# Kernel tuning notes

Measured on AMD Instinct MI355X. Metric: run time of the kernel, lower is better.

Reference implementation:

```python
import jax, jax.numpy as jnp
import numpy as np

NEG_BIG = -1e12
ALPHA = 0.2  # LeakyReLU negative slope

def setup_inputs() -> dict:
    key = jax.random.key(0)
    k1, k2, k3, k4, k5 = jax.random.split(key, 5)
    N, F_in, F_out = 8192, 256, 128
    inp = jax.random.normal(k1, (N, F_in), dtype=jnp.float32)
    adj = jax.random.randint(k2, (N, N), 0, 2, dtype=jnp.int32)
    W = jax.random.normal(k3, (F_in, F_out), dtype=jnp.float32) * 0.05
    W_2 = jax.random.normal(k4, (F_in, F_out), dtype=jnp.float32) * 0.05
    W_3 = jax.random.normal(k5, (F_in, F_out), dtype=jnp.float32) * 0.05
    return {"inp": inp, "adj": adj, "W": W, "W_2": W_2, "W_3": W_3}

def reference(inp, adj, W, W_2, W_3):
    # h = inp @ W, h_2 = inp @ W_2  -> scores e = LeakyReLU(h @ h_2^T)  [N, N]
    h = inp @ W
    h_2 = inp @ W_2
    e = jax.nn.leaky_relu(h @ h_2.T, negative_slope=ALPHA)
    # adjacency mask, row softmax (dropout disabled: eval mode)
    attention = jax.nn.softmax(jnp.where(adj > 0, e, NEG_BIG), axis=1)
    h_3 = inp @ W_3
    h_prime = attention @ h_3
    return jax.nn.elu(h_prime)  # concat=True path
```

## Files before the change

kernel.cpp:

```cpp
#include <hip/hip_runtime.h>
#include <hip/hip_fp16.h>

#define N    8192
#define FIN  256
#define FOUT 128
#define BN   64

typedef _Float16 half8 __attribute__((ext_vector_type(8)));
typedef _Float16 half4v __attribute__((ext_vector_type(4)));
typedef float floatx4 __attribute__((ext_vector_type(4)));

__device__ __forceinline__ float exp2_fast(float x) { return __builtin_amdgcn_exp2f(x); }

__device__ __forceinline__ void gload_lds16(const void* g, void* l) {
    __builtin_amdgcn_global_load_lds(
        (const __attribute__((address_space(1))) void*)g,
        (__attribute__((address_space(3))) void*)l, 16, 0, 0);
}

__global__ __launch_bounds__(256)
void prep_kernel(const float* __restrict__ W0,
                 const float* __restrict__ W1,
                 const float* __restrict__ W2,
                 _Float16* __restrict__ Wf,
                 const int* __restrict__ adj,
                 unsigned long long* __restrict__ adjb)
{
    if (blockIdx.x < 48) {
        int idx  = blockIdx.x * 256 + threadIdx.x;
        int lane = idx & 63;
        int frag = idx >> 6;
        int w    = frag >> 6;
        int f    = frag & 63;
        int nt   = f >> 3, kc = f & 7;
        int quad = lane >> 4, lo16 = lane & 15;
        const float* Wp = w == 0 ? W0 : (w == 1 ? W1 : W2);
        half8 v;
#pragma unroll
        for (int jj = 0; jj < 8; jj++)
            v[jj] = (_Float16)Wp[(size_t)(kc * 32 + quad * 8 + jj) * FOUT + nt * 16 + lo16];
        *(half8*)&Wf[(size_t)idx * 8] = v;
    } else {
        const int gw   = ((blockIdx.x - 48) * 256 + threadIdx.x) >> 6;
        const int lane = threadIdx.x & 63;
        const int NW   = 2048 * 4;
        for (int t = gw; t < N * 32; t += NW) {
            int row = t >> 5, c4 = t & 31;
            const int* p = adj + (size_t)row * N + c4 * 256 + lane;
            int a0 = p[0], a1 = p[64], a2 = p[128], a3 = p[192];
            unsigned long long b0 = __ballot(a0 != 0);
            unsigned long long b1 = __ballot(a1 != 0);
            unsigned long long b2 = __ballot(a2 != 0);
            unsigned long long b3 = __ballot(a3 != 0);
            unsigned long long v = lane == 0 ? b0 : (lane == 1 ? b1 : (lane == 2 ? b2 : b3));
            if (lane < 4) adjb[(size_t)row * (N / 64) + c4 * 4 + lane] = v;
        }
    }
}

__global__ __launch_bounds__(256, 2)
void gemm3_kernel(const float* __restrict__ inp,
                  const _Float16* __restrict__ Wf,
                  _Float16* __restrict__ H,
                  _Float16* __restrict__ H2,
                  _Float16* __restrict__ H3T)
{
    const int which = blockIdx.z;
    const int c0    = blockIdx.y * 64;
    const _Float16* Wfw = Wf + (size_t)which * 64 * 64 * 8;
    const int r0 = blockIdx.x * 64;
    const int tid  = threadIdx.x;
    const int wave = tid >> 6;
    const int lane = tid & 63;
    const int lo16 = lane & 15;
    const int quad = lane >> 4;
    const int r = r0 + wave * 16 + lo16;

    half8 a[8];
#pragma unroll
    for (int kc = 0; kc < 8; kc++) {
        const float* p = &inp[(size_t)r * FIN + kc * 32 + quad * 8];
        float4 v0 = *(const float4*)p;
        float4 v1 = *(const float4*)(p + 4);
        a[kc][0] = (_Float16)v0.x; a[kc][1] = (_Float16)v0.y;
        a[kc][2] = (_Float16)v0.z; a[kc][3] = (_Float16)v0.w;
        a[kc][4] = (_Float16)v1.x; a[kc][5] = (_Float16)v1.y;
        a[kc][6] = (_Float16)v1.z; a[kc][7] = (_Float16)v1.w;
    }

    floatx4 acc[4];
#pragma unroll
    for (int i = 0; i < 4; i++) acc[i] = (floatx4){0.f, 0.f, 0.f, 0.f};

#pragma unroll
    for (int kc = 0; kc < 8; kc++)
#pragma unroll
        for (int nt = 0; nt < 4; nt++) {
            int ntg = (c0 >> 4) + nt;
            half8 b = *(const half8*)&Wfw[(((size_t)ntg * 8 + kc) * 64 + lane) * 8];
            acc[nt] = __builtin_amdgcn_mfma_f32_16x16x32_f16(a[kc], b, acc[nt], 0, 0, 0);
        }

    const int arow = wave * 16 + quad * 4;
    if (which < 2) {
        _Float16* outp = which == 0 ? H : H2;
        const float scale = which == 0 ? 1.44269504f : 1.0f;
#pragma unroll
        for (int nt = 0; nt < 4; nt++)
#pragma unroll
            for (int rr = 0; rr < 4; rr++)
                outp[(size_t)(r0 + arow + rr) * FOUT + c0 + nt * 16 + lo16] =
                    (_Float16)(acc[nt][rr] * scale);
    } else {
#pragma unroll
        for (int nt = 0; nt < 4; nt++) {
            half4v v;
#pragma unroll
            for (int rr = 0; rr < 4; rr++) v[rr] = (_Float16)acc[nt][rr];
            *(half4v*)&H3T[(size_t)(c0 + nt * 16 + lo16) * N + r0 + arow] = v;
        }
    }
}

__global__ __launch_bounds__(256)
void repackKV_kernel(const _Float16* __restrict__ H2,
                     const _Float16* __restrict__ H3T,
                     _Float16* __restrict__ Kf,
                     _Float16* __restrict__ Vf)
{
    if (blockIdx.x < 512) {
        int idx  = blockIdx.x * 256 + threadIdx.x;
        int lane = idx & 63;
        int frag = idx >> 6;
        int jb = frag >> 4, f = frag & 15;
        int c = f >> 3, ntj = (f >> 2) & 1, kc = f & 3;
        int quad = lane >> 4, lo16 = lane & 15;
        int srcrow = jb * 64 + c * 32 + (lo16 >> 2) * 8 + ntj * 4 + (lo16 & 3);
        half8 v = *(const half8*)&H2[(size_t)srcrow * FOUT + kc * 32 + quad * 8];
        *(half8*)&Kf[(size_t)idx * 8] = v;
    } else {
        int idx  = (blockIdx.x - 512) * 256 + threadIdx.x;
        int lane = idx & 63;
        int frag = idx >> 6;
        int jb = frag >> 4, f = frag & 15, nt = f >> 1, kc = f & 1;
        int quad = lane >> 4, lo16 = lane & 15;
        half8 v = *(const half8*)&H3T[(size_t)(nt * 16 + lo16) * N + jb * 64 + kc * 32 + quad * 8];
        *(half8*)&Vf[(size_t)idx * 8] = v;
    }
}

template<int JS>
__global__ __launch_bounds__(256, 2)
void attn_kernel(const _Float16* __restrict__ Hq,
                 const _Float16* __restrict__ Kf,
                 const _Float16* __restrict__ Vf,
                 const unsigned long long* __restrict__ adjb,
                 float* __restrict__ OpartT,
                 float* __restrict__ mpart,
                 float* __restrict__ lpart)
{
    __shared__ __align__(16) _Float16 KV[2][16384];

    const int tid  = threadIdx.x;
    const int wave = tid >> 6;
    const int lane = tid & 63;
    const int lo16 = lane & 15;
    const int quad = lane >> 4;
    const int bid  = blockIdx.x;
    const int js   = bid & (JS - 1);
    const int ib   = bid / JS;
    const int iw   = ib * 128 + wave * 32;
    const int jbeg = js * (N / JS);
    const int NIT  = (N / JS) / BN;

    half8 q[2][4];
#pragma unroll
    for (int isub = 0; isub < 2; isub++)
#pragma unroll
        for (int kc = 0; kc < 4; kc++)
            q[isub][kc] = *(const half8*)&Hq[(size_t)(iw + isub * 16 + lo16) * FOUT + kc * 32 + quad * 8];

    floatx4 O[8][2];
#pragma unroll
    for (int nt = 0; nt < 8; nt++)
#pragma unroll
        for (int s = 0; s < 2; s++) O[nt][s] = (floatx4){0.f, 0.f, 0.f, 0.f};
    float m_s[2] = {-1e12f, -1e12f}, l_s[2] = {0.f, 0.f};

    const unsigned long long* ar0 = adjb + (size_t)(iw + lo16) * (N / 64) + (jbeg >> 6);
    const unsigned long long* ar1 = ar0 + (size_t)16 * (N / 64);

    {
        const int jb0 = jbeg >> 6;
        const _Float16* gk = Kf + (size_t)jb0 * 8192;
        const _Float16* gv = Vf + (size_t)jb0 * 8192;
#pragma unroll
        for (int r = 0; r < 4; r++) {
            int goff = (r * 256 + tid) * 8;
            int loff = (r * 256 + wave * 64) * 8;
            gload_lds16(gk + goff, &KV[0][loff]);
            gload_lds16(gv + goff, &KV[0][8192 + loff]);
        }
        __syncthreads();
    }

    int cur = 0;
    for (int it = 0; it < NIT; it++) {
        if (it + 1 < NIT) {
            const int jbn = (jbeg >> 6) + it + 1;
            const int nxt = cur ^ 1;
            const _Float16* gk = Kf + (size_t)jbn * 8192;
            const _Float16* gv = Vf + (size_t)jbn * 8192;
#pragma unroll
            for (int r = 0; r < 4; r++) {
                int goff = (r * 256 + tid) * 8;
                int loff = (r * 256 + wave * 64) * 8;
                gload_lds16(gk + goff, &KV[nxt][loff]);
                gload_lds16(gv + goff, &KV[nxt][8192 + loff]);
            }
        }

        unsigned long long mw[2] = { ar0[it], ar1[it] };

        const _Float16* kb = &KV[cur][0];
        const _Float16* vb = &KV[cur][8192];

        floatx4 S[2][2][2];
#pragma unroll
        for (int c = 0; c < 2; c++)
#pragma unroll
            for (int ntj = 0; ntj < 2; ntj++) {
                S[c][ntj][0] = (floatx4){0.f, 0.f, 0.f, 0.f};
                S[c][ntj][1] = (floatx4){0.f, 0.f, 0.f, 0.f};
#pragma unroll
                for (int kc = 0; kc < 4; kc++) {
                    half8 kf = *(const half8*)&kb[(((c * 2 + ntj) * 4 + kc) * 64 + lane) * 8];
                    S[c][ntj][0] = __builtin_amdgcn_mfma_f32_16x16x32_f16(kf, q[0][kc], S[c][ntj][0], 0, 0, 0);
                    S[c][ntj][1] = __builtin_amdgcn_mfma_f32_16x16x32_f16(kf, q[1][kc], S[c][ntj][1], 0, 0, 0);
                }
            }

        half8 pb[2][2];
#pragma unroll
        for (int s = 0; s < 2; s++) {
            float mx = -1e12f;
#pragma unroll
            for (int c = 0; c < 2; c++)
#pragma unroll
                for (int ntj = 0; ntj < 2; ntj++)
#pragma unroll
                    for (int r = 0; r < 4; r++) {
                        float e = S[c][ntj][s][r];
                        e = fmaxf(e, 0.2f * e);
                        S[c][ntj][s][r] = e;
                        mx = fmaxf(mx, e);
                    }
            mx = fmaxf(mx, __shfl_xor(mx, 16));
            mx = fmaxf(mx, __shfl_xor(mx, 32));
            if (__any(mx > m_s[s] + 5.75f)) {
                float mn = fmaxf(m_s[s], mx);
                float al = exp2_fast(m_s[s] - mn);
                m_s[s] = mn;
                l_s[s] *= al;
#pragma unroll
                for (int nt = 0; nt < 8; nt++)
#pragma unroll
                    for (int r = 0; r < 4; r++)
                        O[nt][s][r] *= al;
            }

            unsigned long long mq = mw[s] >> (quad * 8);
            unsigned mh[2] = { (unsigned)mq, (unsigned)(mq >> 32) };
            float sum = 0.f;
#pragma unroll
            for (int c = 0; c < 2; c++)
#pragma unroll
                for (int ntj = 0; ntj < 2; ntj++)
#pragma unroll
                    for (int r = 0; r < 4; r++) {
                        float e = S[c][ntj][s][r] - m_s[s];
                        bool bit = (mh[c] >> (ntj * 4 + r)) & 1u;
                        float p = bit ? exp2_fast(e) : 0.f;
                        sum += p;
                        pb[s][c][ntj * 4 + r] = (_Float16)p;
                    }
            sum += __shfl_xor(sum, 16);
            sum += __shfl_xor(sum, 32);
            l_s[s] += sum;
        }

#pragma unroll
        for (int c = 0; c < 2; c++)
#pragma unroll
            for (int nt = 0; nt < 8; nt++) {
                half8 vf = *(const half8*)&vb[((nt * 2 + c) * 64 + lane) * 8];
                O[nt][0] = __builtin_amdgcn_mfma_f32_16x16x32_f16(vf, pb[0][c], O[nt][0], 0, 0, 0);
                O[nt][1] = __builtin_amdgcn_mfma_f32_16x16x32_f16(vf, pb[1][c], O[nt][1], 0, 0, 0);
            }

        __syncthreads();
        cur ^= 1;
    }

#pragma unroll
    for (int nt = 0; nt < 8; nt++)
#pragma unroll
        for (int s = 0; s < 2; s++)
#pragma unroll
            for (int r = 0; r < 4; r++) {
                int f = nt * 16 + quad * 4 + r;
                int i = iw + s * 16 + lo16;
                OpartT[((size_t)js * FOUT + f) * N + i] = O[nt][s][r];
            }
    if (quad == 0) {
#pragma unroll
        for (int s = 0; s < 2; s++) {
            mpart[js * N + iw + s * 16 + lo16] = m_s[s];
            lpart[js * N + iw + s * 16 + lo16] = l_s[s];
        }
    }
}

template<int JS>
__global__ __launch_bounds__(256)
void combine_kernel(const float* __restrict__ OpartT,
                    const float* __restrict__ mpart,
                    const float* __restrict__ lpart,
                    float* __restrict__ out)
{
    int idx = blockIdx.x * 256 + threadIdx.x;
    int f  = idx >> 11;
    int i4 = (idx & 2047) << 2;

    float4 M = {-3e38f, -3e38f, -3e38f, -3e38f};
    float4 m[JS];
#pragma unroll
    for (int s = 0; s < JS; s++) {
        m[s] = *(const float4*)&mpart[s * N + i4];
        M.x = fmaxf(M.x, m[s].x); M.y = fmaxf(M.y, m[s].y);
        M.z = fmaxf(M.z, m[s].z); M.w = fmaxf(M.w, m[s].w);
    }
    float4 L = {0.f, 0.f, 0.f, 0.f};
    float4 w[JS];
#pragma unroll
    for (int s = 0; s < JS; s++) {
        float4 l = *(const float4*)&lpart[s * N + i4];
        w[s].x = exp2_fast(m[s].x - M.x); w[s].y = exp2_fast(m[s].y - M.y);
        w[s].z = exp2_fast(m[s].z - M.z); w[s].w = exp2_fast(m[s].w - M.w);
        L.x += l.x * w[s].x; L.y += l.y * w[s].y;
        L.z += l.z * w[s].z; L.w += l.w * w[s].w;
    }
    float4 o = {0.f, 0.f, 0.f, 0.f};
#pragma unroll
    for (int s = 0; s < JS; s++) {
        float4 v = *(const float4*)&OpartT[((size_t)s * FOUT + f) * N + i4];
        o.x += w[s].x * v.x; o.y += w[s].y * v.y;
        o.z += w[s].z * v.z; o.w += w[s].w * v.w;
    }
    float r0 = o.x / L.x, r1 = o.y / L.y, r2 = o.z / L.z, r3 = o.w / L.w;
    out[(size_t)(i4 + 0) * FOUT + f] = r0 > 0.f ? r0 : __expf(r0) - 1.f;
    out[(size_t)(i4 + 1) * FOUT + f] = r1 > 0.f ? r1 : __expf(r1) - 1.f;
    out[(size_t)(i4 + 2) * FOUT + f] = r2 > 0.f ? r2 : __expf(r2) - 1.f;
    out[(size_t)(i4 + 3) * FOUT + f] = r3 > 0.f ? r3 : __expf(r3) - 1.f;
}

extern "C" void kernel_launch(void* const* d_in, const int* in_sizes, int n_in,
                              void* d_out, int out_size, void* d_ws, size_t ws_size,
                              hipStream_t stream) {
    const float* inp = (const float*)d_in[0];
    const int*   adj = (const int*)d_in[1];
    const float* W0  = (const float*)d_in[2];
    const float* W1  = (const float*)d_in[3];
    const float* W2  = (const float*)d_in[4];
    float* out = (float*)d_out;

    constexpr int JS = 8;
    char* ws = (char*)d_ws;
    _Float16* H    = (_Float16*)(ws);
    _Float16* H2   = (_Float16*)(ws + (2u << 20));
    _Float16* H3T  = (_Float16*)(ws + (4u << 20));
    _Float16* Wf   = (_Float16*)(ws + (6u << 20));
    _Float16* Kf   = (_Float16*)(ws + (7u << 20));
    _Float16* Vf   = (_Float16*)(ws + (9u << 20));
    float* OpartT  = (float*)(ws + (11u << 20));
    float* mpart   = (float*)(ws + (43u << 20));
    float* lpart   = (float*)(ws + (43u << 20) + (size_t)JS * N * sizeof(float));
    unsigned long long* adjb = (unsigned long long*)(ws + (44u << 20));

    prep_kernel<<<2096, 256, 0, stream>>>(W0, W1, W2, Wf, adj, adjb);
    gemm3_kernel<<<dim3(N / 64, 2, 3), 256, 0, stream>>>(inp, Wf, H, H2, H3T);
    repackKV_kernel<<<1024, 256, 0, stream>>>(H2, H3T, Kf, Vf);
    attn_kernel<JS><<<(N / 128) * JS, 256, 0, stream>>>(H, Kf, Vf, adjb, OpartT, mpart, lpart);
    combine_kernel<JS><<<(FOUT * (N / 4)) / 256, 256, 0, stream>>>(OpartT, mpart, lpart, out);
}
```

Measured before the change: 437.3 us.

## Fuse adjacency bit-packing into projection GEMM launch with transposed bitmask layout

Splits the weight prep into its own small kernel and moves adjacency bit-packing into the GEMM launch as extra blocks, so the large adj read overlaps the projection GEMMs. The packed mask is stored transposed (word-column major), so attention waves read 16 consecutive row words per iteration instead of strided rows. The combine loop is also merged into one pass over the splits to cut register pressure. The packing now reads 16 rows per wave with strided loads, which may coalesce less well than the previous row-contiguous pattern.

```diff
diff --git a/kernel.cpp b/kernel.cpp
--- a/kernel.cpp
+++ b/kernel.cpp
@@ -19,56 +19,62 @@
 }
 
 __global__ __launch_bounds__(256)
-void prep_kernel(const float* __restrict__ W0,
-                 const float* __restrict__ W1,
-                 const float* __restrict__ W2,
-                 _Float16* __restrict__ Wf,
-                 const int* __restrict__ adj,
-                 unsigned long long* __restrict__ adjb)
-{
-    if (blockIdx.x < 48) {
-        int idx  = blockIdx.x * 256 + threadIdx.x;
-        int lane = idx & 63;
-        int frag = idx >> 6;
-        int w    = frag >> 6;
-        int f    = frag & 63;
-        int nt   = f >> 3, kc = f & 7;
-        int quad = lane >> 4, lo16 = lane & 15;
-        const float* Wp = w == 0 ? W0 : (w == 1 ? W1 : W2);
-        half8 v;
-#pragma unroll
-        for (int jj = 0; jj < 8; jj++)
-            v[jj] = (_Float16)Wp[(size_t)(kc * 32 + quad * 8 + jj) * FOUT + nt * 16 + lo16];
-        *(half8*)&Wf[(size_t)idx * 8] = v;
-    } else {
-        const int gw   = ((blockIdx.x - 48) * 256 + threadIdx.x) >> 6;
+void wprep_kernel(const float* __restrict__ W0,
+                  const float* __restrict__ W1,
+                  const float* __restrict__ W2,
+                  _Float16* __restrict__ Wf)
+{
+    int idx  = blockIdx.x * 256 + threadIdx.x;
+    int lane = idx & 63;
+    int frag = idx >> 6;
+    int w    = frag >> 6;
+    int f    = frag & 63;
+    int nt   = f >> 3, kc = f & 7;
+    int quad = lane >> 4, lo16 = lane & 15;
+    const float* Wp = w == 0 ? W0 : (w == 1 ? W1 : W2);
+    half8 v;
+#pragma unroll
+    for (int jj = 0; jj < 8; jj++)
+        v[jj] = (_Float16)Wp[(size_t)(kc * 32 + quad * 8 + jj) * FOUT + nt * 16 + lo16];
+    *(half8*)&Wf[(size_t)idx * 8] = v;
+}
+
+__global__ __launch_bounds__(256, 2)
+void gemmadj_kernel(const float* __restrict__ inp,
+                    const _Float16* __restrict__ Wf,
+                    _Float16* __restrict__ H,
+                    _Float16* __restrict__ H2,
+                    _Float16* __restrict__ H3T,
+                    const int* __restrict__ adj,
+                    unsigned long long* __restrict__ adjbT)
+{
+    if (blockIdx.x >= 768) {
+        const int gw   = (blockIdx.x - 768) * 4 + (threadIdx.x >> 6);
         const int lane = threadIdx.x & 63;
-        const int NW   = 2048 * 4;
-        for (int t = gw; t < N * 32; t += NW) {
-            int row = t >> 5, c4 = t & 31;
-            const int* p = adj + (size_t)row * N + c4 * 256 + lane;
-            int a0 = p[0], a1 = p[64], a2 = p[128], a3 = p[192];
-            unsigned long long b0 = __ballot(a0 != 0);
-            unsigned long long b1 = __ballot(a1 != 0);
-            unsigned long long b2 = __ballot(a2 != 0);
-            unsigned long long b3 = __ballot(a3 != 0);
-            unsigned long long v = lane == 0 ? b0 : (lane == 1 ? b1 : (lane == 2 ? b2 : b3));
-            if (lane < 4) adjb[(size_t)row * (N / 64) + c4 * 4 + lane] = v;
-        }
-    }
-}
-
-__global__ __launch_bounds__(256, 2)
-void gemm3_kernel(const float* __restrict__ inp,
-                  const _Float16* __restrict__ Wf,
-                  _Float16* __restrict__ H,
-                  _Float16* __restrict__ H2,
-                  _Float16* __restrict__ H3T)
-{
-    const int which = blockIdx.z;
-    const int c0    = blockIdx.y * 64;
+#pragma unroll 1
+        for (int k = 0; k < 16; k++) {
+            int t  = gw + k * 4096;
+            int w  = t >> 9;
+            int rg = t & 511;
+            const int* p = adj + (size_t)(rg * 16) * N + w * 64 + lane;
+            unsigned long long myw = 0;
+#pragma unroll
+            for (int i = 0; i < 16; i++) {
+                unsigned long long b = __ballot(p[(size_t)i * N] != 0);
+                myw = (lane == i) ? b : myw;
+            }
+            if (lane < 16)
+                adjbT[(size_t)w * N + rg * 16 + lane] = myw;
+        }
+        return;
+    }
+
+    const int g     = blockIdx.x;
+    const int which = g >> 8;
+    const int rem   = g & 255;
+    const int c0    = ((rem >> 7) & 1) * 64;
+    const int r0    = (rem & 127) * 64;
     const _Float16* Wfw = Wf + (size_t)which * 64 * 64 * 8;
-    const int r0 = blockIdx.x * 64;
     const int tid  = threadIdx.x;
     const int wave = tid >> 6;
     const int lane = tid & 63;
@@ -154,7 +160,7 @@
 void attn_kernel(const _Float16* __restrict__ Hq,
                  const _Float16* __restrict__ Kf,
                  const _Float16* __restrict__ Vf,
-                 const unsigned long long* __restrict__ adjb,
+                 const unsigned long long* __restrict__ adjbT,
                  float* __restrict__ OpartT,
                  float* __restrict__ mpart,
                  float* __restrict__ lpart)
@@ -172,6 +178,7 @@
     const int iw   = ib * 128 + wave * 32;
     const int jbeg = js * (N / JS);
     const int NIT  = (N / JS) / BN;
+    const int jb0  = jbeg >> 6;
 
     half8 q[2][4];
 #pragma unroll
@@ -187,11 +194,7 @@
         for (int s = 0; s < 2; s++) O[nt][s] = (floatx4){0.f, 0.f, 0.f, 0.f};
     float m_s[2] = {-1e12f, -1e12f}, l_s[2] = {0.f, 0.f};
 
-    const unsigned long long* ar0 = adjb + (size_t)(iw + lo16) * (N / 64) + (jbeg >> 6);
-    const unsigned long long* ar1 = ar0 + (size_t)16 * (N / 64);
-
     {
-        const int jb0 = jbeg >> 6;
         const _Float16* gk = Kf + (size_t)jb0 * 8192;
         const _Float16* gv = Vf + (size_t)jb0 * 8192;
 #pragma unroll
@@ -207,7 +210,7 @@
     int cur = 0;
     for (int it = 0; it < NIT; it++) {
         if (it + 1 < NIT) {
-            const int jbn = (jbeg >> 6) + it + 1;
+            const int jbn = jb0 + it + 1;
             const int nxt = cur ^ 1;
             const _Float16* gk = Kf + (size_t)jbn * 8192;
             const _Float16* gv = Vf + (size_t)jbn * 8192;
@@ -220,7 +223,8 @@
             }
         }
 
-        unsigned long long mw[2] = { ar0[it], ar1[it] };
+        const unsigned long long* aw = adjbT + (size_t)(jb0 + it) * N + iw;
+        unsigned long long mw[2] = { aw[lo16], aw[16 + lo16] };
 
         const _Float16* kb = &KV[cur][0];
         const _Float16* vb = &KV[cur][8192];
@@ -341,21 +345,18 @@
         M.z = fmaxf(M.z, m[s].z); M.w = fmaxf(M.w, m[s].w);
     }
     float4 L = {0.f, 0.f, 0.f, 0.f};
-    float4 w[JS];
+    float4 o = {0.f, 0.f, 0.f, 0.f};
 #pragma unroll
     for (int s = 0; s < JS; s++) {
         float4 l = *(const float4*)&lpart[s * N + i4];
-        w[s].x = exp2_fast(m[s].x - M.x); w[s].y = exp2_fast(m[s].y - M.y);
-        w[s].z = exp2_fast(m[s].z - M.z); w[s].w = exp2_fast(m[s].w - M.w);
-        L.x += l.x * w[s].x; L.y += l.y * w[s].y;
-        L.z += l.z * w[s].z; L.w += l.w * w[s].w;
-    }
-    float4 o = {0.f, 0.f, 0.f, 0.f};
-#pragma unroll
-    for (int s = 0; s < JS; s++) {
+        float4 w;
+        w.x = exp2_fast(m[s].x - M.x); w.y = exp2_fast(m[s].y - M.y);
+        w.z = exp2_fast(m[s].z - M.z); w.w = exp2_fast(m[s].w - M.w);
+        L.x += l.x * w.x; L.y += l.y * w.y;
+        L.z += l.z * w.z; L.w += l.w * w.w;
         float4 v = *(const float4*)&OpartT[((size_t)s * FOUT + f) * N + i4];
-        o.x += w[s].x * v.x; o.y += w[s].y * v.y;
-        o.z += w[s].z * v.z; o.w += w[s].w * v.w;
+        o.x += w.x * v.x; o.y += w.y * v.y;
+        o.z += w.z * v.z; o.w += w.w * v.w;
     }
     float r0 = o.x / L.x, r1 = o.y / L.y, r2 = o.z / L.z, r3 = o.w / L.w;
     out[(size_t)(i4 + 0) * FOUT + f] = r0 > 0.f ? r0 : __expf(r0) - 1.f;
@@ -385,11 +386,11 @@
     float* OpartT  = (float*)(ws + (11u << 20));
     float* mpart   = (float*)(ws + (43u << 20));
     float* lpart   = (float*)(ws + (43u << 20) + (size_t)JS * N * sizeof(float));
-    unsigned long long* adjb = (unsigned long long*)(ws + (44u << 20));
-
-    prep_kernel<<<2096, 256, 0, stream>>>(W0, W1, W2, Wf, adj, adjb);
-    gemm3_kernel<<<dim3(N / 64, 2, 3), 256, 0, stream>>>(inp, Wf, H, H2, H3T);
+    unsigned long long* adjbT = (unsigned long long*)(ws + (44u << 20));
+
+    wprep_kernel<<<48, 256, 0, stream>>>(W0, W1, W2, Wf);
+    gemmadj_kernel<<<768 + 1024, 256, 0, stream>>>(inp, Wf, H, H2, H3T, adj, adjbT);
     repackKV_kernel<<<1024, 256, 0, stream>>>(H2, H3T, Kf, Vf);
-    attn_kernel<JS><<<(N / 128) * JS, 256, 0, stream>>>(H, Kf, Vf, adjb, OpartT, mpart, lpart);
+    attn_kernel<JS><<<(N / 128) * JS, 256, 0, stream>>>(H, Kf, Vf, adjbT, OpartT, mpart, lpart);
     combine_kernel<JS><<<(FOUT * (N / 4)) / 256, 256, 0, stream>>>(OpartT, mpart, lpart, out);
 }
```

After: 460.9 us. +5.4%, slower.
